# Performance work log

Hardware: AMD Instinct MI355X
Metric: run time of the kernel (lower is better)

Reference implementation:

```python
import jax, jax.numpy as jnp
import numpy as np

START_IDX = 1
STOP_IDX = 2
VOCAB = 32000
EMB = 512
HID = 512


def setup_inputs() -> dict:
    key = jax.random.key(0)
    ks = jax.random.split(key, 10)
    B, T = 64, 50
    x = jax.random.normal(ks[0], (B, HID), dtype=jnp.float32)
    labels = jax.random.randint(ks[1], (B, T), 0, VOCAB, dtype=jnp.int64)
    s = 0.02
    emb = jax.random.normal(ks[2], (VOCAB, EMB), dtype=jnp.float32) * s
    W_ih = jax.random.normal(ks[3], (4 * HID, EMB), dtype=jnp.float32) * s
    W_hh = jax.random.normal(ks[4], (4 * HID, HID), dtype=jnp.float32) * s
    b_ih = jax.random.normal(ks[5], (4 * HID,), dtype=jnp.float32) * s
    b_hh = jax.random.normal(ks[6], (4 * HID,), dtype=jnp.float32) * s
    fc_W = jax.random.normal(ks[7], (VOCAB, HID), dtype=jnp.float32) * s
    fc_b = jax.random.normal(ks[8], (VOCAB,), dtype=jnp.float32) * s
    return {"x": x, "labels": labels, "emb": emb, "W_ih": W_ih, "W_hh": W_hh,
            "b_ih": b_ih, "b_hh": b_hh, "fc_W": fc_W, "fc_b": fc_b}


def _decode_loss(x, labels, emb, W_ih, W_hh, b_ih, b_hh, fc_W, fc_b):
    B, T = labels.shape
    # teacher-forced inputs: [START, y_0..y_{T-1}]; targets: [y_0..y_{T-1}, STOP]
    inputs = jnp.concatenate([jnp.full((B, 1), START_IDX, labels.dtype), labels], axis=1)
    targets = jnp.concatenate([labels, jnp.full((B, 1), STOP_IDX, labels.dtype)], axis=1)
    x_emb = emb[inputs]                       # [B, T+1, E]
    x_emb_t = jnp.swapaxes(x_emb, 0, 1)       # [T+1, B, E]

    def step(carry, xt):
        h, c = carry
        gates = xt @ W_ih.T + b_ih + h @ W_hh.T + b_hh   # [B, 4H]
        i, f, g, o = jnp.split(gates, 4, axis=-1)         # torch gate order i,f,g,o
        i = jax.nn.sigmoid(i); f = jax.nn.sigmoid(f)
        g = jnp.tanh(g); o = jax.nn.sigmoid(o)
        c = f * c + i * g
        h = o * jnp.tanh(c)
        return (h, c), h

    # init_states(x[i]): hidden and cell initialized from image feature
    (_, _), hs = jax.lax.scan(step, (x, x), x_emb_t)      # hs: [T+1, B, H]
    logits = hs @ fc_W.T + fc_b                            # [T+1, B, V]
    logp = jax.nn.log_softmax(logits, axis=-1)
    tgt = jnp.swapaxes(targets, 0, 1)[..., None]           # [T+1, B, 1]
    nll = -jnp.take_along_axis(logp, tgt, axis=-1)         # [T+1, B, 1]
    # original: per-step CrossEntropyLoss on batch of 1, summed over steps, / batch_size
    return nll.sum() / B


def reference(x, labels, emb, W_ih, W_hh, b_ih, b_hh, fc_W, fc_b):
    return _decode_loss(x, labels, emb, W_ih, W_hh, b_ih, b_hh, fc_W, fc_b)
```

## Files before the change

### kernel.cpp

```cpp
#include <hip/hip_runtime.h>
#include <cstddef>
#include <cstdint>

#define B_  64
#define T_  51
#define H_  512
#define G4_ 2048
#define V_  32000
#define R_  (T_ * B_)

typedef __attribute__((ext_vector_type(8))) short bf16x8;
typedef __attribute__((ext_vector_type(4))) float f32x4;
typedef __attribute__((ext_vector_type(4))) unsigned int u32x4;
typedef unsigned long long ull;

__device__ __forceinline__ uint16_t f2bf(float f) {
    uint32_t u = __float_as_uint(f);
    u += 0x7FFFu + ((u >> 16) & 1u);
    return (uint16_t)(u >> 16);
}
__device__ __forceinline__ float bf2f(uint32_t h) { return __uint_as_float(h << 16); }

__device__ __forceinline__ void ldsc(u32x4& d, const uint32_t* p) {
    asm volatile("global_load_dwordx4 %0, %1, off sc0 sc1" : "=v"(d) : "v"(p));
}
__device__ __forceinline__ uint32_t ldflag(const uint32_t* p) {
    uint32_t v;
    asm volatile("global_load_dword %0, %1, off sc0 sc1\n\ts_waitcnt vmcnt(0)"
                 : "=v"(v) : "v"(p));
    return v;
}
__device__ __forceinline__ void stflag(uint32_t* p, uint32_t v) {
    asm volatile("global_store_dword %0, %1, off sc0 sc1" :: "v"(p), "v"(v) : "memory");
}
__device__ __forceinline__ void stsh(uint16_t* p, uint32_t v) {
    asm volatile("global_store_short %0, %1, off sc0 sc1" :: "v"(p), "v"(v) : "memory");
}

__device__ __forceinline__ void gl_lds16(const void* g, void* l) {
    __builtin_amdgcn_global_load_lds((const __attribute__((address_space(1))) void*)g,
                                     (__attribute__((address_space(3))) void*)l, 16, 0, 0);
}

__global__ __launch_bounds__(256) void k0_init(const float* __restrict__ x,
                                               uint16_t* __restrict__ hx,
                                               float* __restrict__ sumexp,
                                               uint32_t* __restrict__ flags) {
    int i = blockIdx.x * 256 + threadIdx.x;
    if (i < B_ * H_) hx[i] = f2bf(x[i]);
    if (i < R_) sumexp[i] = 0.f;
    if (i < T_ * 128) flags[i] = 0;
}

__global__ __launch_bounds__(256) void kcvt(const float* __restrict__ src,
                                            uint16_t* __restrict__ dst, int n8) {
    int i = blockIdx.x * 256 + threadIdx.x;
    if (i >= n8) return;
    const float4* s = (const float4*)src + (size_t)i * 2;
    float4 f0 = s[0], f1 = s[1];
    union { uint16_t h[8]; uint4 u; } p;
    p.h[0]=f2bf(f0.x); p.h[1]=f2bf(f0.y); p.h[2]=f2bf(f0.z); p.h[3]=f2bf(f0.w);
    p.h[4]=f2bf(f1.x); p.h[5]=f2bf(f1.y); p.h[6]=f2bf(f1.z); p.h[7]=f2bf(f1.w);
    ((uint4*)dst)[i] = p.u;
}

template<int CVT>
__global__ __launch_bounds__(256, 2) void k1_mfma(const int* __restrict__ labels,
                                                  const float* __restrict__ emb,
                                                  const void* __restrict__ wih,
                                                  const float* __restrict__ b_ih,
                                                  const float* __restrict__ b_hh,
                                                  uint16_t* __restrict__ XgT) {
    __shared__ uint16_t Al[64 * 72];
    __shared__ uint16_t Bl[256 * 72];
    const int t    = blockIdx.y;
    const int n0   = blockIdx.x * 256;
    const int tid  = threadIdx.x;
    const int w    = tid >> 6;
    const int lane = tid & 63;
    const int l15  = lane & 15;
    const int lhi  = lane >> 4;

    f32x4 acc[4][4];
    #pragma unroll
    for (int mi = 0; mi < 4; ++mi)
        #pragma unroll
        for (int nf = 0; nf < 4; ++nf) acc[mi][nf] = (f32x4){0.f, 0.f, 0.f, 0.f};

    for (int k0 = 0; k0 < H_; k0 += 64) {
        #pragma unroll
        for (int r = 0; r < 2; ++r) {
            int idx = r * 256 + tid, row = idx >> 3, seg = idx & 7;
            int tok = (t == 0) ? 1 : labels[row * 50 + (t - 1)];
            const float* s = emb + (size_t)tok * H_ + k0 + seg * 8;
            float4 f0 = *(const float4*)s;
            float4 f1 = *(const float4*)(s + 4);
            union { uint16_t h[8]; uint4 u; } p;
            p.h[0]=f2bf(f0.x); p.h[1]=f2bf(f0.y); p.h[2]=f2bf(f0.z); p.h[3]=f2bf(f0.w);
            p.h[4]=f2bf(f1.x); p.h[5]=f2bf(f1.y); p.h[6]=f2bf(f1.z); p.h[7]=f2bf(f1.w);
            *(uint4*)(Al + row * 72 + seg * 8) = p.u;
        }
        #pragma unroll
        for (int r = 0; r < 8; ++r) {
            int idx = r * 256 + tid, row = idx >> 3, seg = idx & 7;
            if (CVT) {
                const float* s = (const float*)wih + (size_t)(n0 + row) * H_ + k0 + seg * 8;
                float4 f0 = *(const float4*)s;
                float4 f1 = *(const float4*)(s + 4);
                union { uint16_t h[8]; uint4 u; } p;
                p.h[0]=f2bf(f0.x); p.h[1]=f2bf(f0.y); p.h[2]=f2bf(f0.z); p.h[3]=f2bf(f0.w);
                p.h[4]=f2bf(f1.x); p.h[5]=f2bf(f1.y); p.h[6]=f2bf(f1.z); p.h[7]=f2bf(f1.w);
                *(uint4*)(Bl + row * 72 + seg * 8) = p.u;
            } else {
                *(uint4*)(Bl + row * 72 + seg * 8) =
                    *(const uint4*)((const uint16_t*)wih + (size_t)(n0 + row) * H_ + k0 + seg * 8);
            }
        }
        __syncthreads();
        #pragma unroll
        for (int ks = 0; ks < 2; ++ks) {
            bf16x8 a[4];
            #pragma unroll
            for (int mi = 0; mi < 4; ++mi)
                a[mi] = *(const bf16x8*)(Al + (mi * 16 + l15) * 72 + ks * 32 + lhi * 8);
            #pragma unroll
            for (int nf = 0; nf < 4; ++nf) {
                bf16x8 b = *(const bf16x8*)(Bl + (w * 64 + nf * 16 + l15) * 72 + ks * 32 + lhi * 8);
                #pragma unroll
                for (int mi = 0; mi < 4; ++mi)
                    acc[mi][nf] = __builtin_amdgcn_mfma_f32_16x16x32_bf16(a[mi], b, acc[mi][nf], 0, 0, 0);
            }
        }
        __syncthreads();
    }
    float bias[4];
    #pragma unroll
    for (int nf = 0; nf < 4; ++nf) {
        int col = n0 + w * 64 + nf * 16 + l15;
        bias[nf] = b_ih[col] + b_hh[col];
    }
    #pragma unroll
    for (int mi = 0; mi < 4; ++mi)
        #pragma unroll
        for (int nf = 0; nf < 4; ++nf) {
            const int col = n0 + w * 64 + nf * 16 + l15;
            const int g = col >> 9, u = col & 511;
            const int b = mi * 16 + lhi * 4;
            union { uint16_t h[4]; ull q; } pk;
            #pragma unroll
            for (int q = 0; q < 4; ++q) pk.h[q] = f2bf(acc[mi][nf][q] + bias[nf]);
            *(ull*)(XgT + ((size_t)(t * 512 + u) * 4 + g) * 64 + b) = pk.q;
        }
}

__global__ __launch_bounds__(256, 1) void k2p(const uint16_t* __restrict__ hx,
                                              const float* __restrict__ x,
                                              const uint16_t* __restrict__ XgT,
                                              const float* __restrict__ W_hh,
                                              uint16_t* __restrict__ hs,
                                              uint32_t* __restrict__ flags) {
    __shared__ uint16_t Wl[64 * 520];
    const int tid  = threadIdx.x;
    const int bid  = blockIdx.x;
    const int u0   = bid * 16;
    const int w    = tid >> 6;
    const int lane = tid & 63;
    const int l15  = lane & 15;
    const int lhi  = lane >> 4;
    const int arow = w * 16 + l15;

    {
        const int c = tid >> 2;
        const int q = tid & 3;
        const int j = (c >> 4) * 512 + u0 + (c & 15);
        const float* src = W_hh + (size_t)j * H_ + q * 128;
        uint16_t* dst = Wl + c * 520 + q * 128;
        #pragma unroll
        for (int i = 0; i < 128; i += 8) {
            float4 f0 = *(const float4*)(src + i);
            float4 f1 = *(const float4*)(src + i + 4);
            union { uint16_t h[8]; uint4 u; } p;
            p.h[0]=f2bf(f0.x); p.h[1]=f2bf(f0.y); p.h[2]=f2bf(f0.z); p.h[3]=f2bf(f0.w);
            p.h[4]=f2bf(f1.x); p.h[5]=f2bf(f1.y); p.h[6]=f2bf(f1.z); p.h[7]=f2bf(f1.w);
            *(uint4*)(dst + i) = p.u;
        }
    }
    float cst[4];
    #pragma unroll
    for (int q = 0; q < 4; ++q)
        cst[q] = x[(size_t)(w * 16 + lhi * 4 + q) * H_ + u0 + l15];
    __syncthreads();

    for (int t = 0; t < T_; ++t) {
        ull xgp[4];
        #pragma unroll
        for (int g = 0; g < 4; ++g)
            xgp[g] = *(const ull*)(XgT + ((size_t)(t * 512 + u0 + l15) * 4 + g) * 64 + w * 16 + lhi * 4);

        u32x4 ha[16];
        if (t == 0) {
            const uint16_t* hb = hx + (size_t)arow * H_ + lhi * 8;
            #pragma unroll
            for (int ks = 0; ks < 16; ++ks)
                ha[ks] = *(const u32x4*)(hb + ks * 32);
        } else {
            const uint32_t* fp = flags + (size_t)(t - 1) * 128 + (lane & 31) * 4 + w;
            for (;;) {
                uint32_t fv = 1;
                if (lane < 32) fv = ldflag(fp);
                if (!__any((int)(fv == 0))) break;
            }
            __builtin_amdgcn_sched_barrier(0);
            const uint16_t* hb = hs + ((size_t)(t - 1) * 64 + arow) * H_ + lhi * 8;
            #pragma unroll
            for (int ks = 0; ks < 16; ++ks)
                ldsc(ha[ks], (const uint32_t*)(hb + ks * 32));
        }
        f32x4 acc[4];
        #pragma unroll
        for (int nf = 0; nf < 4; ++nf) acc[nf] = (f32x4){0.f, 0.f, 0.f, 0.f};
        if (t != 0) { asm volatile("s_waitcnt vmcnt(8)" ::: "memory");
                      __builtin_amdgcn_sched_barrier(0); }
        #pragma unroll
        for (int ks = 0; ks < 8; ++ks) {
            union { u32x4 u; bf16x8 v; } au; au.u = ha[ks];
            #pragma unroll
            for (int nf = 0; nf < 4; ++nf) {
                bf16x8 b = *(const bf16x8*)(Wl + (nf * 16 + l15) * 520 + ks * 32 + lhi * 8);
                acc[nf] = __builtin_amdgcn_mfma_f32_16x16x32_bf16(au.v, b, acc[nf], 0, 0, 0);
            }
        }
        if (t != 0) { asm volatile("s_waitcnt vmcnt(0)" ::: "memory");
                      __builtin_amdgcn_sched_barrier(0); }
        #pragma unroll
        for (int ks = 8; ks < 16; ++ks) {
            union { u32x4 u; bf16x8 v; } au; au.u = ha[ks];
            #pragma unroll
            for (int nf = 0; nf < 4; ++nf) {
                bf16x8 b = *(const bf16x8*)(Wl + (nf * 16 + l15) * 520 + ks * 32 + lhi * 8);
                acc[nf] = __builtin_amdgcn_mfma_f32_16x16x32_bf16(au.v, b, acc[nf], 0, 0, 0);
            }
        }
        #pragma unroll
        for (int q = 0; q < 4; ++q) {
            const int b = w * 16 + lhi * 4 + q;
            float gi = acc[0][q] + bf2f((uint32_t)((xgp[0] >> (16 * q)) & 0xFFFF));
            float gf = acc[1][q] + bf2f((uint32_t)((xgp[1] >> (16 * q)) & 0xFFFF));
            float gg = acc[2][q] + bf2f((uint32_t)((xgp[2] >> (16 * q)) & 0xFFFF));
            float go = acc[3][q] + bf2f((uint32_t)((xgp[3] >> (16 * q)) & 0xFFFF));
            float si = 1.f / (1.f + __expf(-gi));
            float sf = 1.f / (1.f + __expf(-gf));
            float tg = tanhf(gg);
            float so = 1.f / (1.f + __expf(-go));
            float cc = sf * cst[q] + si * tg;
            cst[q] = cc;
            stsh(hs + (size_t)(t * 64 + b) * H_ + u0 + l15, (uint32_t)f2bf(so * tanhf(cc)));
        }
        asm volatile("s_waitcnt vmcnt(0)" ::: "memory");
        if (lane == 0) stflag(flags + (size_t)t * 128 + bid * 4 + w, (uint32_t)(t + 1));
    }
}

template<int CVT>
__global__ __launch_bounds__(512, 4) void k3_mfma(const uint16_t* __restrict__ hsb,
                                                  const void* __restrict__ fcw,
                                                  const float* __restrict__ fc_b,
                                                  const int* __restrict__ labels,
                                                  float* __restrict__ sumexp,
                                                  float* __restrict__ tgtlog) {
    __shared__ uint16_t Al[128 * 64];
    __shared__ uint16_t Bl[256 * 64];
    const int flat = blockIdx.x;
    const int xcd  = flat & 7;
    const int slot = flat >> 3;
    const int work = (xcd < 2 ? xcd * 407 : 814 + (xcd - 2) * 406) + slot;
    const int m0   = (work % 26) * 128;
    const int v0   = (work / 26) * 256;
    const int tid  = threadIdx.x;
    const int w    = tid >> 6;
    const int lane = tid & 63;
    const int l15  = lane & 15;
    const int lhi  = lane >> 4;
    const int wm   = w >> 2;
    const int wn   = w & 3;

    f32x4 acc[4][4];
    #pragma unroll
    for (int mi = 0; mi < 4; ++mi)
        #pragma unroll
        for (int nf = 0; nf < 4; ++nf) acc[mi][nf] = (f32x4){0.f, 0.f, 0.f, 0.f};

    const int lrow = lane >> 3;
    const int segp = (lane & 7) ^ lrow;

    for (int k0 = 0; k0 < H_; k0 += 64) {
        #pragma unroll
        for (int r = 0; r < 2; ++r) {
            const int g = w * 2 + r, row0 = g * 8;
            int grow = m0 + row0 + lrow; if (grow >= R_) grow = R_ - 1;
            gl_lds16(hsb + (size_t)grow * H_ + k0 + segp * 8, Al + row0 * 64);
        }
        if (CVT == 0) {
            #pragma unroll
            for (int r = 0; r < 4; ++r) {
                const int g = w * 4 + r, row0 = g * 8;
                gl_lds16((const uint16_t*)fcw + (size_t)(v0 + row0 + lrow) * H_ + k0 + segp * 8,
                         Bl + row0 * 64);
            }
        } else {
            #pragma unroll
            for (int r = 0; r < 4; ++r) {
                int idx = r * 512 + tid, row = idx >> 3, seg = idx & 7;
                const float* s = (const float*)fcw + (size_t)(v0 + row) * H_ + k0 + seg * 8;
                float4 f0 = *(const float4*)s;
                float4 f1 = *(const float4*)(s + 4);
                union { uint16_t h[8]; uint4 u; } p;
                p.h[0]=f2bf(f0.x); p.h[1]=f2bf(f0.y); p.h[2]=f2bf(f0.z); p.h[3]=f2bf(f0.w);
                p.h[4]=f2bf(f1.x); p.h[5]=f2bf(f1.y); p.h[6]=f2bf(f1.z); p.h[7]=f2bf(f1.w);
                *(uint4*)(Bl + row * 64 + (seg ^ (row & 7)) * 8) = p.u;
            }
        }
        __syncthreads();
        #pragma unroll
        for (int ks = 0; ks < 2; ++ks) {
            bf16x8 a[4];
            #pragma unroll
            for (int mi = 0; mi < 4; ++mi) {
                const int ar = wm * 64 + mi * 16 + l15;
                a[mi] = *(const bf16x8*)((const char*)Al + ar * 128 +
                        ((ks * 64 + lhi * 16) ^ ((ar & 7) << 4)));
            }
            #pragma unroll
            for (int nf = 0; nf < 4; ++nf) {
                const int br = wn * 64 + nf * 16 + l15;
                bf16x8 b = *(const bf16x8*)((const char*)Bl + br * 128 +
                           ((ks * 64 + lhi * 16) ^ ((br & 7) << 4)));
                #pragma unroll
                for (int mi = 0; mi < 4; ++mi)
                    acc[mi][nf] = __builtin_amdgcn_mfma_f32_16x16x32_bf16(a[mi], b, acc[mi][nf], 0, 0, 0);
            }
        }
        __syncthreads();
    }
    float bias[4];
    #pragma unroll
    for (int nf = 0; nf < 4; ++nf) bias[nf] = fc_b[v0 + wn * 64 + nf * 16 + l15];
    #pragma unroll
    for (int mi = 0; mi < 4; ++mi) {
        #pragma unroll
        for (int q = 0; q < 4; ++q) {
            const int r = m0 + wm * 64 + mi * 16 + lhi * 4 + q;
            if (r >= R_) continue;
            const int t = r >> 6, b = r & 63;
            const int tgt = (t < 50) ? labels[b * 50 + t] : 2;
            float lsum = 0.f;
            #pragma unroll
            for (int nf = 0; nf < 4; ++nf) {
                const int v = v0 + wn * 64 + nf * 16 + l15;
                float lg = acc[mi][nf][q] + bias[nf];
                lsum += __expf(lg);
                if (v == tgt) tgtlog[r] = lg;
            }
            lsum += __shfl_xor(lsum, 1, 16);
            lsum += __shfl_xor(lsum, 2, 16);
            lsum += __shfl_xor(lsum, 4, 16);
            lsum += __shfl_xor(lsum, 8, 16);
            if (l15 == 0) atomicAdd(&sumexp[r], lsum);
        }
    }
}

__global__ __launch_bounds__(256) void k4_loss(const float* __restrict__ sumexp,
                                               const float* __restrict__ tgtlog,
                                               float* __restrict__ out) {
    __shared__ float red[256];
    float s = 0.f;
    for (int r = threadIdx.x; r < R_; r += 256) s += logf(sumexp[r]) - tgtlog[r];
    red[threadIdx.x] = s;
    __syncthreads();
    for (int st = 128; st > 0; st >>= 1) {
        if (threadIdx.x < st) red[threadIdx.x] += red[threadIdx.x + st];
        __syncthreads();
    }
    if (threadIdx.x == 0) out[0] = red[0] / 64.0f;
}

extern "C" void kernel_launch(void* const* d_in, const int* in_sizes, int n_in,
                              void* d_out, int out_size, void* d_ws, size_t ws_size,
                              hipStream_t stream) {
    const float* x      = (const float*)d_in[0];
    const int*   labels = (const int*)d_in[1];
    const float* emb    = (const float*)d_in[2];
    const float* W_ih   = (const float*)d_in[3];
    const float* W_hh   = (const float*)d_in[4];
    const float* b_ih   = (const float*)d_in[5];
    const float* b_hh   = (const float*)d_in[6];
    const float* fc_W   = (const float*)d_in[7];
    const float* fc_b   = (const float*)d_in[8];
    float* out = (float*)d_out;

    char* p = (char*)d_ws;
    uint16_t* XgT    = (uint16_t*)p;  p += (size_t)T_ * 512 * 4 * 64 * 2;
    uint16_t* hsb    = (uint16_t*)p;  p += (size_t)R_ * H_ * 2;
    uint16_t* hx     = (uint16_t*)p;  p += (size_t)B_ * H_ * 2;
    float*    sumexp = (float*)p;     p += (size_t)R_ * 4;
    float*    tgtl   = (float*)p;     p += (size_t)R_ * 4;
    uint32_t* flags  = (uint32_t*)p;  p += (size_t)T_ * 128 * 4 + 256;
    uint16_t* fcwb   = (uint16_t*)p;  p += (size_t)V_ * H_ * 2;
    uint16_t* wihb   = (uint16_t*)p;  p += (size_t)G4_ * H_ * 2;
    const bool pre = ((size_t)(p - (char*)d_ws) <= ws_size);

    k0_init<<<128, 256, 0, stream>>>(x, hx, sumexp, flags);
    if (pre) {
        kcvt<<<8000, 256, 0, stream>>>(fc_W, fcwb, (V_ * H_) / 8);
        kcvt<<<512, 256, 0, stream>>>(W_ih, wihb, (G4_ * H_) / 8);
        k1_mfma<0><<<dim3(8, 51), 256, 0, stream>>>(labels, emb, wihb, b_ih, b_hh, XgT);
    } else {
        k1_mfma<1><<<dim3(8, 51), 256, 0, stream>>>(labels, emb, W_ih, b_ih, b_hh, XgT);
    }
    k2p<<<32, 256, 0, stream>>>(hx, x, XgT, W_hh, hsb, flags);
    if (pre) k3_mfma<0><<<3250, 512, 0, stream>>>(hsb, fcwb, fc_b, labels, sumexp, tgtl);
    else     k3_mfma<1><<<3250, 512, 0, stream>>>(hsb, fc_W, fc_b, labels, sumexp, tgtl);
    k4_loss<<<1, 256, 0, stream>>>(sumexp, tgtl, out);
}
```

Measured before the change: 508.3 us.

## Fuse input-gate GEMM and fc_W conversion into persistent recurrent kernel with flags

Merges the input-projection GEMM, the fc_W bf16 conversion and the LSTM recurrence into one 256-block launch. Blocks 0-31 run the recurrence and poll per-timestep readiness flags that the other 224 blocks set after writing each XgT tile, then those blocks convert fc_W in the background. W_ih is now converted on the fly and x is converted inside the recurrence, so the separate hx init and W_ih conversion passes are dropped. The aim is to hide the input-projection and conversion work behind the latency-bound serial recurrence and cut launch overhead. The cost is extra flag polling, contention between recurrence blocks and background blocks, and reliance on all 256 blocks being co-resident so the spin-wait cannot deadlock.

```diff
diff --git a/kernel.cpp b/kernel.cpp
--- a/kernel.cpp
+++ b/kernel.cpp
@@ -8,6 +8,7 @@
 #define G4_ 2048
 #define V_  32000
 #define R_  (T_ * B_)
+#define NHF (T_ * 128)
 
 typedef __attribute__((ext_vector_type(8))) short bf16x8;
 typedef __attribute__((ext_vector_type(4))) float f32x4;
@@ -23,6 +24,9 @@
 
 __device__ __forceinline__ void ldsc(u32x4& d, const uint32_t* p) {
     asm volatile("global_load_dwordx4 %0, %1, off sc0 sc1" : "=v"(d) : "v"(p));
+}
+__device__ __forceinline__ void ldq2(ull& d, const uint16_t* p) {
+    asm volatile("global_load_dwordx2 %0, %1, off sc0 sc1" : "=v"(d) : "v"(p));
 }
 __device__ __forceinline__ uint32_t ldflag(const uint32_t* p) {
     uint32_t v;
@@ -36,139 +40,134 @@
 __device__ __forceinline__ void stsh(uint16_t* p, uint32_t v) {
     asm volatile("global_store_short %0, %1, off sc0 sc1" :: "v"(p), "v"(v) : "memory");
 }
+__device__ __forceinline__ void stq(uint16_t* p, ull v) {
+    asm volatile("global_store_dwordx2 %0, %1, off sc0 sc1" :: "v"(p), "v"(v) : "memory");
+}
 
 __device__ __forceinline__ void gl_lds16(const void* g, void* l) {
     __builtin_amdgcn_global_load_lds((const __attribute__((address_space(1))) void*)g,
                                      (__attribute__((address_space(3))) void*)l, 16, 0, 0);
 }
 
-__global__ __launch_bounds__(256) void k0_init(const float* __restrict__ x,
-                                               uint16_t* __restrict__ hx,
-                                               float* __restrict__ sumexp,
+__global__ __launch_bounds__(256) void k0_init(float* __restrict__ sumexp,
                                                uint32_t* __restrict__ flags) {
     int i = blockIdx.x * 256 + threadIdx.x;
-    if (i < B_ * H_) hx[i] = f2bf(x[i]);
     if (i < R_) sumexp[i] = 0.f;
-    if (i < T_ * 128) flags[i] = 0;
-}
-
-__global__ __launch_bounds__(256) void kcvt(const float* __restrict__ src,
-                                            uint16_t* __restrict__ dst, int n8) {
-    int i = blockIdx.x * 256 + threadIdx.x;
-    if (i >= n8) return;
-    const float4* s = (const float4*)src + (size_t)i * 2;
-    float4 f0 = s[0], f1 = s[1];
-    union { uint16_t h[8]; uint4 u; } p;
-    p.h[0]=f2bf(f0.x); p.h[1]=f2bf(f0.y); p.h[2]=f2bf(f0.z); p.h[3]=f2bf(f0.w);
-    p.h[4]=f2bf(f1.x); p.h[5]=f2bf(f1.y); p.h[6]=f2bf(f1.z); p.h[7]=f2bf(f1.w);
-    ((uint4*)dst)[i] = p.u;
-}
-
-template<int CVT>
-__global__ __launch_bounds__(256, 2) void k1_mfma(const int* __restrict__ labels,
-                                                  const float* __restrict__ emb,
-                                                  const void* __restrict__ wih,
-                                                  const float* __restrict__ b_ih,
-                                                  const float* __restrict__ b_hh,
-                                                  uint16_t* __restrict__ XgT) {
-    __shared__ uint16_t Al[64 * 72];
-    __shared__ uint16_t Bl[256 * 72];
-    const int t    = blockIdx.y;
-    const int n0   = blockIdx.x * 256;
+    if (i < NHF + 512) flags[i] = 0;
+}
+
+template<int DOFC>
+__global__ __launch_bounds__(256) void k12p(const float* __restrict__ x,
+                                            const int* __restrict__ labels,
+                                            const float* __restrict__ emb,
+                                            const float* __restrict__ W_ih,
+                                            const float* __restrict__ b_ih,
+                                            const float* __restrict__ b_hh,
+                                            const float* __restrict__ W_hh,
+                                            const float* __restrict__ fc_W,
+                                            uint16_t* __restrict__ fcwb,
+                                            uint16_t* __restrict__ XgT,
+                                            uint16_t* __restrict__ hs,
+                                            uint32_t* __restrict__ flags) {
+    __shared__ uint16_t smem[64 * 520];
+    const int bid  = blockIdx.x;
     const int tid  = threadIdx.x;
     const int w    = tid >> 6;
     const int lane = tid & 63;
     const int l15  = lane & 15;
     const int lhi  = lane >> 4;
 
-    f32x4 acc[4][4];
-    #pragma unroll
-    for (int mi = 0; mi < 4; ++mi)
-        #pragma unroll
-        for (int nf = 0; nf < 4; ++nf) acc[mi][nf] = (f32x4){0.f, 0.f, 0.f, 0.f};
-
-    for (int k0 = 0; k0 < H_; k0 += 64) {
-        #pragma unroll
-        for (int r = 0; r < 2; ++r) {
-            int idx = r * 256 + tid, row = idx >> 3, seg = idx & 7;
-            int tok = (t == 0) ? 1 : labels[row * 50 + (t - 1)];
-            const float* s = emb + (size_t)tok * H_ + k0 + seg * 8;
-            float4 f0 = *(const float4*)s;
-            float4 f1 = *(const float4*)(s + 4);
-            union { uint16_t h[8]; uint4 u; } p;
-            p.h[0]=f2bf(f0.x); p.h[1]=f2bf(f0.y); p.h[2]=f2bf(f0.z); p.h[3]=f2bf(f0.w);
-            p.h[4]=f2bf(f1.x); p.h[5]=f2bf(f1.y); p.h[6]=f2bf(f1.z); p.h[7]=f2bf(f1.w);
-            *(uint4*)(Al + row * 72 + seg * 8) = p.u;
-        }
-        #pragma unroll
-        for (int r = 0; r < 8; ++r) {
-            int idx = r * 256 + tid, row = idx >> 3, seg = idx & 7;
-            if (CVT) {
-                const float* s = (const float*)wih + (size_t)(n0 + row) * H_ + k0 + seg * 8;
-                float4 f0 = *(const float4*)s;
-                float4 f1 = *(const float4*)(s + 4);
+    if (bid >= 32) {
+        uint16_t* Al = smem;
+        uint16_t* Bl = smem + 64 * 72;
+        for (int id = bid - 32; id < 408; id += 224) {
+            const int t  = id >> 3;
+            const int n0 = (id & 7) * 256;
+            f32x4 acc[4][4];
+            #pragma unroll
+            for (int mi = 0; mi < 4; ++mi)
+                #pragma unroll
+                for (int nf = 0; nf < 4; ++nf) acc[mi][nf] = (f32x4){0.f, 0.f, 0.f, 0.f};
+            for (int k0 = 0; k0 < H_; k0 += 64) {
+                #pragma unroll
+                for (int r = 0; r < 2; ++r) {
+                    int idx = r * 256 + tid, row = idx >> 3, seg = idx & 7;
+                    int tok = (t == 0) ? 1 : labels[row * 50 + (t - 1)];
+                    const float* s = emb + (size_t)tok * H_ + k0 + seg * 8;
+                    float4 f0 = *(const float4*)s;
+                    float4 f1 = *(const float4*)(s + 4);
+                    union { uint16_t h[8]; uint4 u; } p;
+                    p.h[0]=f2bf(f0.x); p.h[1]=f2bf(f0.y); p.h[2]=f2bf(f0.z); p.h[3]=f2bf(f0.w);
+                    p.h[4]=f2bf(f1.x); p.h[5]=f2bf(f1.y); p.h[6]=f2bf(f1.z); p.h[7]=f2bf(f1.w);
+                    *(uint4*)(Al + row * 72 + seg * 8) = p.u;
+                }
+                #pragma unroll
+                for (int r = 0; r < 8; ++r) {
+                    int idx = r * 256 + tid, row = idx >> 3, seg = idx & 7;
+                    const float* s = W_ih + (size_t)(n0 + row) * H_ + k0 + seg * 8;
+                    float4 f0 = *(const float4*)s;
+                    float4 f1 = *(const float4*)(s + 4);
+                    union { uint16_t h[8]; uint4 u; } p;
+                    p.h[0]=f2bf(f0.x); p.h[1]=f2bf(f0.y); p.h[2]=f2bf(f0.z); p.h[3]=f2bf(f0.w);
+                    p.h[4]=f2bf(f1.x); p.h[5]=f2bf(f1.y); p.h[6]=f2bf(f1.z); p.h[7]=f2bf(f1.w);
+                    *(uint4*)(Bl + row * 72 + seg * 8) = p.u;
+                }
+                __syncthreads();
+                #pragma unroll
+                for (int ks = 0; ks < 2; ++ks) {
+                    bf16x8 a[4];
+                    #pragma unroll
+                    for (int mi = 0; mi < 4; ++mi)
+                        a[mi] = *(const bf16x8*)(Al + (mi * 16 + l15) * 72 + ks * 32 + lhi * 8);
+                    #pragma unroll
+                    for (int nf = 0; nf < 4; ++nf) {
+                        bf16x8 b = *(const bf16x8*)(Bl + (w * 64 + nf * 16 + l15) * 72 + ks * 32 + lhi * 8);
+                        #pragma unroll
+                        for (int mi = 0; mi < 4; ++mi)
+                            acc[mi][nf] = __builtin_amdgcn_mfma_f32_16x16x32_bf16(a[mi], b, acc[mi][nf], 0, 0, 0);
+                    }
+                }
+                __syncthreads();
+            }
+            float bias[4];
+            #pragma unroll
+            for (int nf = 0; nf < 4; ++nf) {
+                int col = n0 + w * 64 + nf * 16 + l15;
+                bias[nf] = b_ih[col] + b_hh[col];
+            }
+            #pragma unroll
+            for (int mi = 0; mi < 4; ++mi)
+                #pragma unroll
+                for (int nf = 0; nf < 4; ++nf) {
+                    const int col = n0 + w * 64 + nf * 16 + l15;
+                    const int g = col >> 9, u = col & 511;
+                    const int b = mi * 16 + lhi * 4;
+                    union { uint16_t h[4]; ull q; } pk;
+                    #pragma unroll
+                    for (int q = 0; q < 4; ++q) pk.h[q] = f2bf(acc[mi][nf][q] + bias[nf]);
+                    stq(XgT + ((size_t)(t * 512 + u) * 4 + g) * 64 + b, pk.q);
+                }
+            asm volatile("s_waitcnt vmcnt(0)" ::: "memory");
+            __syncthreads();
+            if (tid == 0) stflag(flags + NHF + t * 8 + (n0 >> 8), 1u);
+        }
+        if (DOFC) {
+            const int n8 = (V_ * H_) / 8;
+            for (int i = (bid - 32) * 256 + tid; i < n8; i += 224 * 256) {
+                const float4* s = (const float4*)fc_W + (size_t)i * 2;
+                float4 f0 = s[0], f1 = s[1];
                 union { uint16_t h[8]; uint4 u; } p;
                 p.h[0]=f2bf(f0.x); p.h[1]=f2bf(f0.y); p.h[2]=f2bf(f0.z); p.h[3]=f2bf(f0.w);
                 p.h[4]=f2bf(f1.x); p.h[5]=f2bf(f1.y); p.h[6]=f2bf(f1.z); p.h[7]=f2bf(f1.w);
-                *(uint4*)(Bl + row * 72 + seg * 8) = p.u;
-            } else {
-                *(uint4*)(Bl + row * 72 + seg * 8) =
-                    *(const uint4*)((const uint16_t*)wih + (size_t)(n0 + row) * H_ + k0 + seg * 8);
-            }
-        }
-        __syncthreads();
-        #pragma unroll
-        for (int ks = 0; ks < 2; ++ks) {
-            bf16x8 a[4];
-            #pragma unroll
-            for (int mi = 0; mi < 4; ++mi)
-                a[mi] = *(const bf16x8*)(Al + (mi * 16 + l15) * 72 + ks * 32 + lhi * 8);
-            #pragma unroll
-            for (int nf = 0; nf < 4; ++nf) {
-                bf16x8 b = *(const bf16x8*)(Bl + (w * 64 + nf * 16 + l15) * 72 + ks * 32 + lhi * 8);
-                #pragma unroll
-                for (int mi = 0; mi < 4; ++mi)
-                    acc[mi][nf] = __builtin_amdgcn_mfma_f32_16x16x32_bf16(a[mi], b, acc[mi][nf], 0, 0, 0);
-            }
-        }
-        __syncthreads();
-    }
-    float bias[4];
-    #pragma unroll
-    for (int nf = 0; nf < 4; ++nf) {
-        int col = n0 + w * 64 + nf * 16 + l15;
-        bias[nf] = b_ih[col] + b_hh[col];
-    }
-    #pragma unroll
-    for (int mi = 0; mi < 4; ++mi)
-        #pragma unroll
-        for (int nf = 0; nf < 4; ++nf) {
-            const int col = n0 + w * 64 + nf * 16 + l15;
-            const int g = col >> 9, u = col & 511;
-            const int b = mi * 16 + lhi * 4;
-            union { uint16_t h[4]; ull q; } pk;
-            #pragma unroll
-            for (int q = 0; q < 4; ++q) pk.h[q] = f2bf(acc[mi][nf][q] + bias[nf]);
-            *(ull*)(XgT + ((size_t)(t * 512 + u) * 4 + g) * 64 + b) = pk.q;
-        }
-}
-
-__global__ __launch_bounds__(256, 1) void k2p(const uint16_t* __restrict__ hx,
-                                              const float* __restrict__ x,
-                                              const uint16_t* __restrict__ XgT,
-                                              const float* __restrict__ W_hh,
-                                              uint16_t* __restrict__ hs,
-                                              uint32_t* __restrict__ flags) {
-    __shared__ uint16_t Wl[64 * 520];
-    const int tid  = threadIdx.x;
-    const int bid  = blockIdx.x;
+                ((uint4*)fcwb)[i] = p.u;
+            }
+        }
+        return;
+    }
+
+    uint16_t* Wl = smem;
     const int u0   = bid * 16;
-    const int w    = tid >> 6;
-    const int lane = tid & 63;
-    const int l15  = lane & 15;
-    const int lhi  = lane >> 4;
     const int arow = w * 16 + l15;
-
     {
         const int c = tid >> 2;
         const int q = tid & 3;
@@ -192,34 +191,46 @@
     __syncthreads();
 
     for (int t = 0; t < T_; ++t) {
+        const uint32_t* fp = flags;
+        bool dopoll = false;
+        if (t > 0 && lane < 32)      { fp = flags + (size_t)(t - 1) * 128 + lane * 4 + w; dopoll = true; }
+        else if (lane >= 32 && lane < 40) { fp = flags + NHF + t * 8 + (lane - 32); dopoll = true; }
+        else if (t == 0 && lane < 8) { fp = flags + NHF + (lane); dopoll = true; }
+        for (;;) {
+            uint32_t fv = 1;
+            if (dopoll) fv = ldflag(fp);
+            if (!__any((int)(fv == 0))) break;
+            __builtin_amdgcn_s_sleep(1);
+        }
+        __builtin_amdgcn_sched_barrier(0);
+
+        u32x4 ha[16];
         ull xgp[4];
-        #pragma unroll
-        for (int g = 0; g < 4; ++g)
-            xgp[g] = *(const ull*)(XgT + ((size_t)(t * 512 + u0 + l15) * 4 + g) * 64 + w * 16 + lhi * 4);
-
-        u32x4 ha[16];
         if (t == 0) {
-            const uint16_t* hb = hx + (size_t)arow * H_ + lhi * 8;
-            #pragma unroll
-            for (int ks = 0; ks < 16; ++ks)
-                ha[ks] = *(const u32x4*)(hb + ks * 32);
+            const float* xb = x + (size_t)arow * H_ + lhi * 8;
+            #pragma unroll
+            for (int ks = 0; ks < 16; ++ks) {
+                float4 f0 = *(const float4*)(xb + ks * 32);
+                float4 f1 = *(const float4*)(xb + ks * 32 + 4);
+                union { uint16_t h[8]; u32x4 u; } p;
+                p.h[0]=f2bf(f0.x); p.h[1]=f2bf(f0.y); p.h[2]=f2bf(f0.z); p.h[3]=f2bf(f0.w);
+                p.h[4]=f2bf(f1.x); p.h[5]=f2bf(f1.y); p.h[6]=f2bf(f1.z); p.h[7]=f2bf(f1.w);
+                ha[ks] = p.u;
+            }
         } else {
-            const uint32_t* fp = flags + (size_t)(t - 1) * 128 + (lane & 31) * 4 + w;
-            for (;;) {
-                uint32_t fv = 1;
-                if (lane < 32) fv = ldflag(fp);
-                if (!__any((int)(fv == 0))) break;
-            }
-            __builtin_amdgcn_sched_barrier(0);
             const uint16_t* hb = hs + ((size_t)(t - 1) * 64 + arow) * H_ + lhi * 8;
             #pragma unroll
             for (int ks = 0; ks < 16; ++ks)
                 ldsc(ha[ks], (const uint32_t*)(hb + ks * 32));
         }
+        #pragma unroll
+        for (int g = 0; g < 4; ++g)
+            ldq2(xgp[g], XgT + ((size_t)(t * 512 + u0 + l15) * 4 + g) * 64 + w * 16 + lhi * 4);
+
         f32x4 acc[4];
         #pragma unroll
         for (int nf = 0; nf < 4; ++nf) acc[nf] = (f32x4){0.f, 0.f, 0.f, 0.f};
-        if (t != 0) { asm volatile("s_waitcnt vmcnt(8)" ::: "memory");
+        if (t != 0) { asm volatile("s_waitcnt vmcnt(12)" ::: "memory");
                       __builtin_amdgcn_sched_barrier(0); }
         #pragma unroll
         for (int ks = 0; ks < 8; ++ks) {
@@ -230,8 +241,8 @@
                 acc[nf] = __builtin_amdgcn_mfma_f32_16x16x32_bf16(au.v, b, acc[nf], 0, 0, 0);
             }
         }
-        if (t != 0) { asm volatile("s_waitcnt vmcnt(0)" ::: "memory");
-                      __builtin_amdgcn_sched_barrier(0); }
+        asm volatile("s_waitcnt vmcnt(0)" ::: "memory");
+        __builtin_amdgcn_sched_barrier(0);
         #pragma unroll
         for (int ks = 8; ks < 16; ++ks) {
             union { u32x4 u; bf16x8 v; } au; au.u = ha[ks];
@@ -402,24 +413,21 @@
     char* p = (char*)d_ws;
     uint16_t* XgT    = (uint16_t*)p;  p += (size_t)T_ * 512 * 4 * 64 * 2;
     uint16_t* hsb    = (uint16_t*)p;  p += (size_t)R_ * H_ * 2;
-    uint16_t* hx     = (uint16_t*)p;  p += (size_t)B_ * H_ * 2;
     float*    sumexp = (float*)p;     p += (size_t)R_ * 4;
     float*    tgtl   = (float*)p;     p += (size_t)R_ * 4;
-    uint32_t* flags  = (uint32_t*)p;  p += (size_t)T_ * 128 * 4 + 256;
+    uint32_t* flags  = (uint32_t*)p;  p += (size_t)(NHF + 512) * 4;
     uint16_t* fcwb   = (uint16_t*)p;  p += (size_t)V_ * H_ * 2;
-    uint16_t* wihb   = (uint16_t*)p;  p += (size_t)G4_ * H_ * 2;
     const bool pre = ((size_t)(p - (char*)d_ws) <= ws_size);
 
-    k0_init<<<128, 256, 0, stream>>>(x, hx, sumexp, flags);
+    k0_init<<<32, 256, 0, stream>>>(sumexp, flags);
     if (pre) {
-        kcvt<<<8000, 256, 0, stream>>>(fc_W, fcwb, (V_ * H_) / 8);
-        kcvt<<<512, 256, 0, stream>>>(W_ih, wihb, (G4_ * H_) / 8);
-        k1_mfma<0><<<dim3(8, 51), 256, 0, stream>>>(labels, emb, wihb, b_ih, b_hh, XgT);
+        k12p<1><<<256, 256, 0, stream>>>(x, labels, emb, W_ih, b_ih, b_hh, W_hh,
+                                         fc_W, fcwb, XgT, hsb, flags);
+        k3_mfma<0><<<3250, 512, 0, stream>>>(hsb, fcwb, fc_b, labels, sumexp, tgtl);
     } else {
-        k1_mfma<1><<<dim3(8, 51), 256, 0, stream>>>(labels, emb, W_ih, b_ih, b_hh, XgT);
-    }
-    k2p<<<32, 256, 0, stream>>>(hx, x, XgT, W_hh, hsb, flags);
-    if (pre) k3_mfma<0><<<3250, 512, 0, stream>>>(hsb, fcwb, fc_b, labels, sumexp, tgtl);
-    else     k3_mfma<1><<<3250, 512, 0, stream>>>(hsb, fc_W, fc_b, labels, sumexp, tgtl);
+        k12p<0><<<256, 256, 0, stream>>>(x, labels, emb, W_ih, b_ih, b_hh, W_hh,
+                                         fc_W, fcwb, XgT, hsb, flags);
+        k3_mfma<1><<<3250, 512, 0, stream>>>(hsb, fc_W, fc_b, labels, sumexp, tgtl);
+    }
     k4_loss<<<1, 256, 0, stream>>>(sumexp, tgtl, out);
 }
```

New measurement: 508.1 us. Within noise of the previous version (-0.0%).
